# Performance work log

Measured on AMD Instinct MI355X. Metric: run time of the kernel, lower is better.

## Reference

```python
import jax, jax.numpy as jnp
import numpy as np

B, D, H, W = 4, 64, 64, 64
MODES = 8
WIDTH = 32
N_LAYERS = 4


def setup_inputs() -> dict:
    key = jax.random.key(0)
    ks = jax.random.split(key, 20)
    C = WIDTH
    m = MODES
    spec_scale = 1.0 / (C * C)
    inp = {
        "velocity_model": jax.random.normal(ks[0], (B, 1, D, H, W), jnp.float32),
        "partial_travel_time": jax.random.normal(ks[1], (B, 1, D, H, W), jnp.float32),
        "lift_w": jax.random.normal(ks[2], (2, C), jnp.float32) * 0.5,
        "lift_b": jax.random.normal(ks[3], (C,), jnp.float32) * 0.1,
        "spec_wr": jax.random.normal(ks[4], (N_LAYERS, 4, C, C, m, m, m), jnp.float32) * spec_scale,
        "spec_wi": jax.random.normal(ks[5], (N_LAYERS, 4, C, C, m, m, m), jnp.float32) * spec_scale,
        "skip_w": jax.random.normal(ks[6], (N_LAYERS, C, C), jnp.float32) * (1.0 / np.sqrt(C)),
        "skip_b": jax.random.normal(ks[7], (N_LAYERS, C), jnp.float32) * 0.1,
        "proj_w": jax.random.normal(ks[8], (C, C), jnp.float32) * (1.0 / np.sqrt(C)),
        "proj_b": jax.random.normal(ks[9], (C,), jnp.float32) * 0.1,
        "fc1_w": jax.random.normal(ks[10], (C, 128), jnp.float32) * (1.0 / np.sqrt(C)),
        "fc1_b": jax.random.normal(ks[11], (128,), jnp.float32) * 0.1,
        "fc2_w": jax.random.normal(ks[12], (128, 64), jnp.float32) * (1.0 / np.sqrt(128)),
        "fc2_b": jax.random.normal(ks[13], (64,), jnp.float32) * 0.1,
        "fc3_w": jax.random.normal(ks[14], (64, 3), jnp.float32) * (1.0 / np.sqrt(64)),
        "fc3_b": jax.random.normal(ks[15], (3,), jnp.float32) * 0.1,
    }
    return inp


def _spectral_conv3d(x, wr, wi, m):
    # x: [B, Cin, D, H, W] real; wr/wi: [4, Cin, Cout, m, m, m]
    b, ci, d, h, w = x.shape
    co = wr.shape[2]
    xf = jnp.fft.rfftn(x, axes=(-3, -2, -1))  # [B, Cin, D, H, W//2+1] complex
    wc = wr + 1j * wi
    lo = slice(None, m)
    hi = slice(-m, None)
    corners = [(lo, lo), (lo, hi), (hi, lo), (hi, hi)]
    out = jnp.zeros((b, co, d, h, w // 2 + 1), dtype=xf.dtype)
    for i, (sd, sh) in enumerate(corners):
        blk = jnp.einsum('bixyz,ioxyz->boxyz', xf[:, :, sd, sh, :m], wc[i])
        out = out.at[:, :, sd, sh, :m].set(blk)
    return jnp.fft.irfftn(out, s=(d, h, w), axes=(-3, -2, -1))


def _channel_linear(x, w, bias):
    # x: [B, Cin, D, H, W]; w: [Cin, Cout]
    return jnp.einsum('bixyz,io->boxyz', x, w) + bias[None, :, None, None, None]


def reference(velocity_model, partial_travel_time, lift_w, lift_b, spec_wr, spec_wi,
              skip_w, skip_b, proj_w, proj_b, fc1_w, fc1_b, fc2_w, fc2_b, fc3_w, fc3_b):
    # concat along channel dim -> [B, 2, D, H, W]
    x = jnp.concatenate([velocity_model, partial_travel_time], axis=1)
    # lifting to hidden width
    x = _channel_linear(x, lift_w, lift_b)
    n_layers = spec_wr.shape[0]
    for l in range(n_layers):
        y = _spectral_conv3d(x, spec_wr[l], spec_wi[l], MODES)
        s = _channel_linear(x, skip_w[l], skip_b[l])
        x = y + s
        if l < n_layers - 1:
            x = jax.nn.gelu(x)
    # projection to out_channels = width
    x = _channel_linear(x, proj_w, proj_b)
    # global spatial mean -> [B, width]
    x = jnp.mean(x, axis=(-3, -2, -1))
    # MLP head: width -> 128 -> 64 -> 3
    x = jax.nn.relu(x @ fc1_w + fc1_b)
    x = jax.nn.relu(x @ fc2_w + fc2_b)
    return x @ fc3_w + fc3_b
```

## Files before the change

kernel.cpp:

```cpp
#include <hip/hip_runtime.h>
#include <math.h>

#define NSP 262144
static constexpr float TWO_PI_OVER_64 = 0.09817477042468103f;

__global__ __launch_bounds__(256) void k_fwd_wh2(const float* __restrict__ vel,
                                                 const float* __restrict__ ptt,
                                                 float2* __restrict__ VP2) {
  __shared__ float plane[64][65];
  __shared__ float2 A[64][8];
  __shared__ float2 tw[64];
  int t = threadIdx.x;
  if (t < 64) { float s, c; sincosf(TWO_PI_OVER_64 * t, &s, &c); tw[t] = make_float2(c, s); }
  int b = blockIdx.x >> 7, ch = (blockIdx.x >> 6) & 1, d = blockIdx.x & 63;
  const float4* src = (const float4*)((ch ? ptt : vel) + (size_t)b * NSP + d * 4096);
  for (int p = 0; p < 4; ++p) {
    int i = t + 256 * p;
    float4 v = src[i];
    int h = i >> 4, sg = (i & 15) * 4;
    plane[h][sg] = v.x; plane[h][sg + 1] = v.y; plane[h][sg + 2] = v.z; plane[h][sg + 3] = v.w;
  }
  __syncthreads();
  for (int p = 0; p < 2; ++p) {
    int o = t + 256 * p;
    int h = o >> 3, kw = o & 7;
    float re = 0.f, im = 0.f;
    for (int w = 0; w < 64; ++w) {
      float2 cs = tw[(kw * w) & 63];
      float v = plane[h][w];
      re += v * cs.x; im -= v * cs.y;
    }
    A[h][kw] = make_float2(re, im);
  }
  __syncthreads();
  if (t < 128) {
    int kh = t >> 3, kw = t & 7;
    int f = (kh < 8) ? kh : kh + 48;
    float re = 0.f, im = 0.f;
    for (int h = 0; h < 64; ++h) {
      float2 cs = tw[(h * f) & 63];
      float2 a = A[h][kw];
      re += a.x * cs.x + a.y * cs.y;
      im += a.y * cs.x - a.x * cs.y;
    }
    VP2[(size_t)blockIdx.x * 128 + t] = make_float2(re, im);
  }
}

__global__ __launch_bounds__(256) void k_fwd_d_lift(const float2* __restrict__ VP2,
                                                    const float* __restrict__ lw,
                                                    const float* __restrict__ lb,
                                                    float2* __restrict__ X3) {
  __shared__ float2 tile[2][64][8];
  __shared__ float2 F[2][16][8];
  __shared__ float2 tw[64];
  int t = threadIdx.x;
  if (t < 64) { float s, c; sincosf(TWO_PI_OVER_64 * t, &s, &c); tw[t] = make_float2(c, s); }
  int b = blockIdx.x >> 4, kh = blockIdx.x & 15;
  for (int p = 0; p < 4; ++p) {
    int i = t + 256 * p;
    int ch = i >> 9, dd = (i >> 3) & 63, kw = i & 7;
    tile[ch][dd][kw] = VP2[(size_t)((b * 2 + ch) * 64 + dd) * 128 + kh * 8 + kw];
  }
  __syncthreads();
  { int ch = t >> 7, kd = (t >> 3) & 15, kw = t & 7;
    int f = (kd < 8) ? kd : kd + 48;
    float re = 0.f, im = 0.f;
    for (int dd = 0; dd < 64; ++dd) {
      float2 cs = tw[(dd * f) & 63];
      float2 v = tile[ch][dd][kw];
      re += v.x * cs.x + v.y * cs.y;
      im += v.y * cs.x - v.x * cs.y;
    }
    F[ch][kd][kw] = make_float2(re, im); }
  __syncthreads();
  for (int p = 0; p < 16; ++p) {
    int o = t + 256 * p;
    int ci = o >> 7, kd = (o >> 3) & 15, kw = o & 7;
    float2 f0 = F[0][kd][kw], f1 = F[1][kd][kw];
    float w0 = lw[ci], w1 = lw[32 + ci];
    float2 v = make_float2(w0 * f0.x + w1 * f1.x, w0 * f0.y + w1 * f1.y);
    if (kh == 0 && kd == 0 && kw == 0) v.x += lb[ci] * 262144.f;
    X3[(size_t)(b * 32 + ci) * 2048 + kd * 128 + kh * 8 + kw] = v;
  }
}

__global__ __launch_bounds__(128) void k_fwd_h(const float2* __restrict__ X1,
                                               float2* __restrict__ X2) {
  __shared__ float2 tile[64][8];
  __shared__ float2 tw[64];
  int t = threadIdx.x;
  if (t < 64) { float s, c; sincosf(TWO_PI_OVER_64 * t, &s, &c); tw[t] = make_float2(c, s); }
  const float4* s4 = (const float4*)(X1 + (size_t)blockIdx.x * 512);
  float4* t4 = (float4*)tile;
  t4[t] = s4[t];
  t4[t + 128] = s4[t + 128];
  __syncthreads();
  int kh = t >> 3, k = t & 7;
  int f = (kh < 8) ? kh : kh + 48;
  float2 E = tw[f];
  float2 cur = make_float2(1.f, 0.f);
  float re = 0.f, im = 0.f;
#pragma unroll 8
  for (int h = 0; h < 64; ++h) {
    float2 v = tile[h][k];
    re += v.x * cur.x + v.y * cur.y;
    im += v.y * cur.x - v.x * cur.y;
    float cx = cur.x * E.x - cur.y * E.y;
    cur.y = cur.x * E.y + cur.y * E.x;
    cur.x = cx;
  }
  X2[(size_t)blockIdx.x * 128 + t] = make_float2(re, im);
}

__global__ __launch_bounds__(128) void k_fwd_d(const float2* __restrict__ X2,
                                               float2* __restrict__ X3) {
  __shared__ float2 tile[64][8];
  __shared__ float2 tw[64];
  int t = threadIdx.x;
  if (t < 64) { float s, c; sincosf(TWO_PI_OVER_64 * t, &s, &c); tw[t] = make_float2(c, s); }
  int kh = blockIdx.x & 15, bc = blockIdx.x >> 4;
  const float2* src = X2 + (size_t)bc * 8192 + kh * 8;
  for (int i = t; i < 512; i += 128) tile[i >> 3][i & 7] = src[(i >> 3) * 128 + (i & 7)];
  __syncthreads();
  int kd = t >> 3, k = t & 7;
  int f = (kd < 8) ? kd : kd + 48;
  float2 E = tw[f];
  float2 cur = make_float2(1.f, 0.f);
  float re = 0.f, im = 0.f;
#pragma unroll 8
  for (int d = 0; d < 64; ++d) {
    float2 v = tile[d][k];
    re += v.x * cur.x + v.y * cur.y;
    im += v.y * cur.x - v.x * cur.y;
    float cx = cur.x * E.x - cur.y * E.y;
    cur.y = cur.x * E.y + cur.y * E.x;
    cur.x = cx;
  }
  X3[(size_t)bc * 2048 + kd * 128 + kh * 8 + k] = make_float2(re, im);
}

__global__ __launch_bounds__(256) void k_mix(const float2* __restrict__ X3,
                                             const float* __restrict__ wr,
                                             const float* __restrict__ wi,
                                             float2* __restrict__ Y3) {
  __shared__ float2 xs[4][32][8];
  int t = threadIdx.x;
  int kd = blockIdx.x >> 4, kh = blockIdx.x & 15;
  for (int i = t; i < 1024; i += 256) {
    int b = i >> 8, ci = (i >> 3) & 31, k = i & 7;
    xs[b][ci][k] = X3[(size_t)(b * 32 + ci) * 2048 + kd * 128 + kh * 8 + k];
  }
  __syncthreads();
  int corner = ((kd >= 8) ? 2 : 0) + ((kh >= 8) ? 1 : 0);
  int md = kd & 7, mh = kh & 7;
  int co = t >> 3, k = t & 7;
  size_t wbase = (size_t)corner * 32 * 32 * 512 + (size_t)md * 64 + (size_t)mh * 8 + k;
  float ar0 = 0, ai0 = 0, ar1 = 0, ai1 = 0, ar2 = 0, ai2 = 0, ar3 = 0, ai3 = 0;
  for (int ci = 0; ci < 32; ++ci) {
    size_t o = wbase + (size_t)(ci * 32 + co) * 512;
    float wre = wr[o], wim = wi[o];
    float2 v0 = xs[0][ci][k], v1 = xs[1][ci][k];
    float2 v2 = xs[2][ci][k], v3 = xs[3][ci][k];
    ar0 += v0.x * wre - v0.y * wim;  ai0 += v0.x * wim + v0.y * wre;
    ar1 += v1.x * wre - v1.y * wim;  ai1 += v1.x * wim + v1.y * wre;
    ar2 += v2.x * wre - v2.y * wim;  ai2 += v2.x * wim + v2.y * wre;
    ar3 += v3.x * wre - v3.y * wim;  ai3 += v3.x * wim + v3.y * wre;
  }
  size_t obase = (size_t)kd * 128 + kh * 8 + k;
  Y3[(size_t)(0 * 32 + co) * 2048 + obase] = make_float2(ar0, ai0);
  Y3[(size_t)(1 * 32 + co) * 2048 + obase] = make_float2(ar1, ai1);
  Y3[(size_t)(2 * 32 + co) * 2048 + obase] = make_float2(ar2, ai2);
  Y3[(size_t)(3 * 32 + co) * 2048 + obase] = make_float2(ar3, ai3);
}

__global__ __launch_bounds__(256) void k_inv_dh(const float2* __restrict__ Y3,
                                                float2* __restrict__ Z2) {
  __shared__ float2 yt[2048];
  __shared__ float2 zd[4][16][8];
  __shared__ float2 tw[64];
  int t = threadIdx.x;
  if (t < 64) { float s, c; sincosf(TWO_PI_OVER_64 * t, &s, &c); tw[t] = make_float2(c, s); }
  int bc = blockIdx.x >> 4, d0 = (blockIdx.x & 15) * 4;
  const float4* y4 = (const float4*)(Y3 + (size_t)bc * 2048);
  float4* yt4 = (float4*)yt;
  for (int p = 0; p < 4; ++p) yt4[t + 256 * p] = y4[t + 256 * p];
  __syncthreads();
  const float sc = 1.f / 262144.f;
  for (int p = 0; p < 2; ++p) {
    int o = t + 256 * p;
    int dd = o >> 7, kh = (o >> 3) & 15, kw = o & 7;
    int d = d0 + dd;
    float re = 0.f, im = 0.f;
#pragma unroll
    for (int kd = 0; kd < 16; ++kd) {
      int f = (kd < 8) ? kd : kd + 48;
      float2 cs = tw[(d * f) & 63];
      float2 v = yt[kd * 128 + kh * 8 + kw];
      re += v.x * cs.x - v.y * cs.y;
      im += v.x * cs.y + v.y * cs.x;
    }
    zd[dd][kh][kw] = make_float2(re * sc, im * sc);
  }
  __syncthreads();
  for (int p = 0; p < 8; ++p) {
    int o = t + 256 * p;
    int dd = o >> 9, h = (o >> 3) & 63, kw = o & 7;
    float re = 0.f, im = 0.f;
#pragma unroll
    for (int kh = 0; kh < 16; ++kh) {
      int f = (kh < 8) ? kh : kh + 48;
      float2 cs = tw[(h * f) & 63];
      float2 v = zd[dd][kh][kw];
      re += v.x * cs.x - v.y * cs.y;
      im += v.x * cs.y + v.y * cs.x;
    }
    Z2[((size_t)bc * 64 + d0 + dd) * 512 + h * 8 + kw] = make_float2(re, im);
  }
}

template <int MODE>
__global__ __launch_bounds__(256, 4) void k_tail(
    const float2* __restrict__ S, const float* __restrict__ xin,
    const float* __restrict__ pttin, const float* __restrict__ lw,
    const float* __restrict__ lb, const float* __restrict__ skw,
    const float* __restrict__ skb, float* __restrict__ xout,
    float2* __restrict__ Sout, float* __restrict__ pr) {
  __shared__ float2 tws[64];
  __shared__ float2 zt[32][2][9];
  __shared__ float sw[(MODE == 0) ? 3 : 32][32];
  __shared__ float xt[(MODE == 0) ? 2 : 32][2][64];
  int t = threadIdx.x;
  if (t < 64) { float s, c; sincosf(TWO_PI_OVER_64 * t, &s, &c); tws[t] = make_float2(c, s); }
  int b = blockIdx.x >> 11, d = (blockIdx.x >> 5) & 63, h0 = (blockIdx.x & 31) * 2;
  {
    int co = t >> 3, hh = (t >> 2) & 1, q = t & 3;
    const float4* S4 = (const float4*)S;
    float4 v = S4[(size_t)((b * 32 + co) * 64 + d) * 256 + (h0 + hh) * 4 + q];
    zt[co][hh][2 * q] = make_float2(v.x, v.y);
    zt[co][hh][2 * q + 1] = make_float2(v.z, v.w);
  }
  if constexpr (MODE == 0) {
    if (t < 64) {
      int ch = t >> 5, hh = (t >> 4) & 1, sg = t & 15;
      const float4* src = (const float4*)(ch ? pttin : xin);
      *(float4*)&xt[ch][hh][sg * 4] =
          src[((size_t)b * NSP + d * 4096 + (h0 + hh) * 64) / 4 + sg];
    } else if (t >= 128 && t < 192) {
      int j = (t >> 5) & 1, co = t & 31;
      float a = 0.f;
      for (int ci = 0; ci < 32; ++ci) a += lw[j * 32 + ci] * skw[ci * 32 + co];
      sw[j][co] = a;
    } else if (t >= 192 && t < 224) {
      int co = t & 31;
      float a = skb[co];
      for (int ci = 0; ci < 32; ++ci) a += lb[ci] * skw[ci * 32 + co];
      sw[2][co] = a;
    }
  } else {
    { int ci = t >> 3, q = t & 7;
      *(float4*)&sw[ci][q * 4] = ((const float4*)skw)[t]; }
    for (int p = 0; p < 4; ++p) {
      int idx = t + 256 * p, row = idx >> 4, ci = row >> 1, hh = row & 1, sg = idx & 15;
      *(float4*)&xt[ci][hh][sg * 4] =
          ((const float4*)xin)[(size_t)(((b * 32 + ci) * 64 + d) * 64 + h0 + hh) * 16 + sg];
    }
  }
  __syncthreads();

  int co = t >> 3, ws = t & 7;
  float2 e1[8];
#pragma unroll
  for (int j = 0; j < 8; ++j) e1[j] = tws[8 * ws + j];
  float bias = (MODE == 0) ? sw[2][co] : skb[co];

  float acc[2][8];
  {
    float z00 = zt[co][0][0].x, z10 = zt[co][1][0].x;
#pragma unroll
    for (int j = 0; j < 8; ++j) { acc[0][j] = bias + z00; acc[1][j] = bias + z10; }
  }
  {
    float2 cur[8];
#pragma unroll
    for (int j = 0; j < 8; ++j) cur[j] = e1[j];
#pragma unroll
    for (int k = 1; k < 8; ++k) {
      float2 z0 = zt[co][0][k], z1 = zt[co][1][k];
#pragma unroll
      for (int j = 0; j < 8; ++j) {
        acc[0][j] += 2.f * (z0.x * cur[j].x - z0.y * cur[j].y);
        acc[1][j] += 2.f * (z1.x * cur[j].x - z1.y * cur[j].y);
      }
      if (k < 7)
#pragma unroll
        for (int j = 0; j < 8; ++j) {
          float cx = cur[j].x * e1[j].x - cur[j].y * e1[j].y;
          cur[j].y = cur[j].x * e1[j].y + cur[j].y * e1[j].x;
          cur[j].x = cx;
        }
    }
  }
  constexpr int NCI = (MODE == 0) ? 2 : 32;
#pragma unroll 4
  for (int ci = 0; ci < NCI; ++ci) {
    float s = sw[ci][co];
#pragma unroll
    for (int hh = 0; hh < 2; ++hh) {
      float4 xa = *(const float4*)&xt[ci][hh][8 * ws];
      float4 xb = *(const float4*)&xt[ci][hh][8 * ws + 4];
      acc[hh][0] += xa.x * s;  acc[hh][1] += xa.y * s;
      acc[hh][2] += xa.z * s;  acc[hh][3] += xa.w * s;
      acc[hh][4] += xb.x * s;  acc[hh][5] += xb.y * s;
      acc[hh][6] += xb.z * s;  acc[hh][7] += xb.w * s;
    }
  }
#pragma unroll
  for (int hh = 0; hh < 2; ++hh)
#pragma unroll
    for (int j = 0; j < 8; ++j) {
      float v = acc[hh][j];
      float u = 0.7978845608028654f * (v + 0.044715f * v * v * v);
      acc[hh][j] = __fdividef(v, 1.f + __expf(-2.f * u));
    }

  if constexpr (MODE == 2) {
    float s = 0.f;
#pragma unroll
    for (int hh = 0; hh < 2; ++hh)
#pragma unroll
      for (int j = 0; j < 8; ++j) s += acc[hh][j];
    s += __shfl_down(s, 4, 8);
    s += __shfl_down(s, 2, 8);
    s += __shfl_down(s, 1, 8);
    if (ws == 0) atomicAdd(&pr[b * 32 + co], s);
  } else {
    float4* x4o = (float4*)xout;
#pragma unroll
    for (int hh = 0; hh < 2; ++hh) {
      size_t o = (((size_t)(b * 32 + co) * 64 + d) * 64 + h0 + hh) * 16 + 2 * ws;
      x4o[o]     = make_float4(acc[hh][0], acc[hh][1], acc[hh][2], acc[hh][3]);
      x4o[o + 1] = make_float4(acc[hh][4], acc[hh][5], acc[hh][6], acc[hh][7]);
    }
    float2 P[2][8];
#pragma unroll
    for (int hh = 0; hh < 2; ++hh)
#pragma unroll
      for (int kw = 0; kw < 8; ++kw) P[hh][kw] = make_float2(0.f, 0.f);
#pragma unroll
    for (int j = 0; j < 8; ++j) {
      float2 cc = make_float2(e1[j].x, -e1[j].y);
      float2 cur = make_float2(1.f, 0.f);
      float g0 = acc[0][j], g1 = acc[1][j];
#pragma unroll
      for (int kw = 0; kw < 8; ++kw) {
        P[0][kw].x += g0 * cur.x;  P[0][kw].y += g0 * cur.y;
        P[1][kw].x += g1 * cur.x;  P[1][kw].y += g1 * cur.y;
        if (kw < 7) {
          float cx = cur.x * cc.x - cur.y * cc.y;
          cur.y = cur.x * cc.y + cur.y * cc.x;
          cur.x = cx;
        }
      }
    }
    float2 Q[2][4];
#pragma unroll
    for (int hh = 0; hh < 2; ++hh)
#pragma unroll
      for (int kk = 0; kk < 4; ++kk) {
        float2 keep = (ws & 4) ? P[hh][kk + 4] : P[hh][kk];
        float2 send = (ws & 4) ? P[hh][kk] : P[hh][kk + 4];
        keep.x += __shfl_xor(send.x, 4);
        keep.y += __shfl_xor(send.y, 4);
        Q[hh][kk] = keep;
      }
    float2 R[2][2];
#pragma unroll
    for (int hh = 0; hh < 2; ++hh)
#pragma unroll
      for (int kk = 0; kk < 2; ++kk) {
        float2 keep = (ws & 2) ? Q[hh][kk + 2] : Q[hh][kk];
        float2 send = (ws & 2) ? Q[hh][kk] : Q[hh][kk + 2];
        keep.x += __shfl_xor(send.x, 2);
        keep.y += __shfl_xor(send.y, 2);
        R[hh][kk] = keep;
      }
#pragma unroll
    for (int hh = 0; hh < 2; ++hh) {
      float2 keep = (ws & 1) ? R[hh][1] : R[hh][0];
      float2 send = (ws & 1) ? R[hh][0] : R[hh][1];
      keep.x += __shfl_xor(send.x, 1);
      keep.y += __shfl_xor(send.y, 1);
      Sout[((size_t)(b * 32 + co) * 64 + d) * 512 + (h0 + hh) * 8 + ws] = keep;
    }
  }
}

__global__ __launch_bounds__(128) void k_head(const float* __restrict__ pr,
                                              const float* __restrict__ swr,
                                              const float* __restrict__ skw,
                                              const float* __restrict__ skb,
                                              const float* __restrict__ pw,
                                              const float* __restrict__ pb,
                                              const float* __restrict__ f1w,
                                              const float* __restrict__ f1b,
                                              const float* __restrict__ f2w,
                                              const float* __restrict__ f2b,
                                              const float* __restrict__ f3w,
                                              const float* __restrict__ f3b,
                                              float* __restrict__ out) {
  __shared__ float m[128], h1[128], p2[128], f1[512], f2[256];
  int t = threadIdx.x;
  m[t] = pr[t] * (1.f / 262144.f);
  __syncthreads();
  { int b = t >> 5, co = t & 31;
    float acc = skb[96 + co];
    for (int ci = 0; ci < 32; ++ci) {
      float wdc = swr[((size_t)12 * 1024 + (size_t)(ci * 32 + co)) * 512];
      acc += m[b * 32 + ci] * (wdc + skw[3072 + ci * 32 + co]);
    }
    h1[t] = acc; }
  __syncthreads();
  { int b = t >> 5, o = t & 31;
    float acc = pb[o];
    for (int c = 0; c < 32; ++c) acc += h1[b * 32 + c] * pw[c * 32 + o];
    p2[t] = acc; }
  __syncthreads();
  for (int j = 0; j < 4; ++j) {
    int idx = t + 128 * j, b = idx >> 7, o = idx & 127;
    float acc = f1b[o];
    for (int c = 0; c < 32; ++c) acc += p2[b * 32 + c] * f1w[c * 128 + o];
    f1[idx] = fmaxf(acc, 0.f);
  }
  __syncthreads();
  for (int j = 0; j < 2; ++j) {
    int idx = t + 128 * j, b = idx >> 6, o = idx & 63;
    float acc = f2b[o];
    for (int c = 0; c < 128; ++c) acc += f1[b * 128 + c] * f2w[c * 64 + o];
    f2[idx] = fmaxf(acc, 0.f);
  }
  __syncthreads();
  if (t < 12) {
    int b = t / 3, o = t % 3;
    float acc = f3b[o];
    for (int c = 0; c < 64; ++c) acc += f2[b * 64 + c] * f3w[c * 3 + o];
    out[t] = acc;
  }
}

extern "C" void kernel_launch(void* const* d_in, const int* in_sizes, int n_in,
                              void* d_out, int out_size, void* d_ws, size_t ws_size,
                              hipStream_t stream) {
  const float* vel = (const float*)d_in[0];
  const float* ptt = (const float*)d_in[1];
  const float* lw  = (const float*)d_in[2];
  const float* lb  = (const float*)d_in[3];
  const float* swr = (const float*)d_in[4];
  const float* swi = (const float*)d_in[5];
  const float* skw = (const float*)d_in[6];
  const float* skb = (const float*)d_in[7];
  const float* pw  = (const float*)d_in[8];
  const float* pb  = (const float*)d_in[9];
  const float* f1w = (const float*)d_in[10];
  const float* f1b = (const float*)d_in[11];
  const float* f2w = (const float*)d_in[12];
  const float* f2b = (const float*)d_in[13];
  const float* f3w = (const float*)d_in[14];
  const float* f3b = (const float*)d_in[15];
  float* out = (float*)d_out;

  char* ws = (char*)d_ws;
  float*  x   = (float*)(ws);
  float2* S   = (float2*)(ws + 134217728ULL);
  float2* X2  = (float2*)(ws + 167772160ULL);
  float2* VP2 = X2;
  float2* X3  = (float2*)(ws + 176160768ULL);
  float2* Y3  = (float2*)(ws + 178257920ULL);
  float*  pr  = (float*)(ws + 180355072ULL);
  if (ws_size < 180355584ULL) return;

  hipMemsetAsync(pr, 0, 512, stream);

  k_fwd_wh2<<<512, 256, 0, stream>>>(vel, ptt, VP2);
  k_fwd_d_lift<<<64, 256, 0, stream>>>(VP2, lw, lb, X3);
  k_mix<<<256, 256, 0, stream>>>(X3, swr, swi, Y3);
  k_inv_dh<<<2048, 256, 0, stream>>>(Y3, S);
  k_tail<0><<<8192, 256, 0, stream>>>(S, vel, ptt, lw, lb, skw, skb, x, S, nullptr);

  k_fwd_h<<<8192, 128, 0, stream>>>(S, X2);
  k_fwd_d<<<2048, 128, 0, stream>>>(X2, X3);
  k_mix<<<256, 256, 0, stream>>>(X3, swr + 2097152, swi + 2097152, Y3);
  k_inv_dh<<<2048, 256, 0, stream>>>(Y3, S);
  k_tail<1><<<8192, 256, 0, stream>>>(S, x, nullptr, nullptr, nullptr,
                                      skw + 1024, skb + 32, x, S, nullptr);

  k_fwd_h<<<8192, 128, 0, stream>>>(S, X2);
  k_fwd_d<<<2048, 128, 0, stream>>>(X2, X3);
  k_mix<<<256, 256, 0, stream>>>(X3, swr + 2 * 2097152, swi + 2 * 2097152, Y3);
  k_inv_dh<<<2048, 256, 0, stream>>>(Y3, S);
  k_tail<2><<<8192, 256, 0, stream>>>(S, x, nullptr, nullptr, nullptr,
                                      skw + 2048, skb + 64, nullptr, nullptr, pr);

  k_head<<<1, 128, 0, stream>>>(pr, swr, skw, skb, pw, pb, f1w, f1b,
                                f2w, f2b, f3w, f3b, out);
}
```

Measured before the change: 738.1 us.

## Register-block k_tail over four output channels and use twiddle table lookups in forward DFTs

k_tail now runs 128 threads per block, with each thread computing four output channels for one h row instead of one channel for two rows. This reuses the x tile and twiddle values across more accumulators and halves the thread count. The forward H and D DFT kernels swap their recurrence-based twiddle rotation for direct shared-memory table lookups, which removes a serial dependency chain. The larger per-thread accumulator set raises register pressure, and the lower occupancy hint (3) may reduce latency hiding.

After: 1.015 ms. +37.5%, slower.

```diff
diff --git a/kernel.cpp b/kernel.cpp
--- a/kernel.cpp
+++ b/kernel.cpp
@@ -98,17 +98,13 @@
   __syncthreads();
   int kh = t >> 3, k = t & 7;
   int f = (kh < 8) ? kh : kh + 48;
-  float2 E = tw[f];
-  float2 cur = make_float2(1.f, 0.f);
   float re = 0.f, im = 0.f;
 #pragma unroll 8
   for (int h = 0; h < 64; ++h) {
+    float2 cs = tw[(h * f) & 63];
     float2 v = tile[h][k];
-    re += v.x * cur.x + v.y * cur.y;
-    im += v.y * cur.x - v.x * cur.y;
-    float cx = cur.x * E.x - cur.y * E.y;
-    cur.y = cur.x * E.y + cur.y * E.x;
-    cur.x = cx;
+    re += v.x * cs.x + v.y * cs.y;
+    im += v.y * cs.x - v.x * cs.y;
   }
   X2[(size_t)blockIdx.x * 128 + t] = make_float2(re, im);
 }
@@ -125,17 +121,13 @@
   __syncthreads();
   int kd = t >> 3, k = t & 7;
   int f = (kd < 8) ? kd : kd + 48;
-  float2 E = tw[f];
-  float2 cur = make_float2(1.f, 0.f);
   float re = 0.f, im = 0.f;
 #pragma unroll 8
   for (int d = 0; d < 64; ++d) {
+    float2 cs = tw[(d * f) & 63];
     float2 v = tile[d][k];
-    re += v.x * cur.x + v.y * cur.y;
-    im += v.y * cur.x - v.x * cur.y;
-    float cx = cur.x * E.x - cur.y * E.y;
-    cur.y = cur.x * E.y + cur.y * E.x;
-    cur.x = cx;
+    re += v.x * cs.x + v.y * cs.y;
+    im += v.y * cs.x - v.x * cs.y;
   }
   X3[(size_t)bc * 2048 + kd * 128 + kh * 8 + k] = make_float2(re, im);
 }
@@ -220,7 +212,7 @@
 }
 
 template <int MODE>
-__global__ __launch_bounds__(256, 4) void k_tail(
+__global__ __launch_bounds__(128, 3) void k_tail(
     const float2* __restrict__ S, const float* __restrict__ xin,
     const float* __restrict__ pttin, const float* __restrict__ lw,
     const float* __restrict__ lb, const float* __restrict__ skw,
@@ -234,11 +226,15 @@
   if (t < 64) { float s, c; sincosf(TWO_PI_OVER_64 * t, &s, &c); tws[t] = make_float2(c, s); }
   int b = blockIdx.x >> 11, d = (blockIdx.x >> 5) & 63, h0 = (blockIdx.x & 31) * 2;
   {
-    int co = t >> 3, hh = (t >> 2) & 1, q = t & 3;
+    int co = t >> 2, sub = t & 3;
     const float4* S4 = (const float4*)S;
-    float4 v = S4[(size_t)((b * 32 + co) * 64 + d) * 256 + (h0 + hh) * 4 + q];
-    zt[co][hh][2 * q] = make_float2(v.x, v.y);
-    zt[co][hh][2 * q + 1] = make_float2(v.z, v.w);
+    size_t base = (size_t)((b * 32 + co) * 64 + d) * 256;
+#pragma unroll
+    for (int hh = 0; hh < 2; ++hh) {
+      float4 v = S4[base + (h0 + hh) * 4 + sub];
+      zt[co][hh][2 * sub] = make_float2(v.x, v.y);
+      zt[co][hh][2 * sub + 1] = make_float2(v.z, v.w);
+    }
   }
   if constexpr (MODE == 0) {
     if (t < 64) {
@@ -246,39 +242,47 @@
       const float4* src = (const float4*)(ch ? pttin : xin);
       *(float4*)&xt[ch][hh][sg * 4] =
           src[((size_t)b * NSP + d * 4096 + (h0 + hh) * 64) / 4 + sg];
-    } else if (t >= 128 && t < 192) {
-      int j = (t >> 5) & 1, co = t & 31;
-      float a = 0.f;
-      for (int ci = 0; ci < 32; ++ci) a += lw[j * 32 + ci] * skw[ci * 32 + co];
-      sw[j][co] = a;
-    } else if (t >= 192 && t < 224) {
-      int co = t & 31;
-      float a = skb[co];
-      for (int ci = 0; ci < 32; ++ci) a += lb[ci] * skw[ci * 32 + co];
-      sw[2][co] = a;
+    } else {
+      for (int i = t - 64; i < 96; i += 64) {
+        int r = i >> 5, co = i & 31;
+        if (r < 2) {
+          float a = 0.f;
+          for (int ci = 0; ci < 32; ++ci) a += lw[r * 32 + ci] * skw[ci * 32 + co];
+          sw[r][co] = a;
+        } else {
+          float a = skb[co];
+          for (int ci = 0; ci < 32; ++ci) a += lb[ci] * skw[ci * 32 + co];
+          sw[2][co] = a;
+        }
+      }
     }
   } else {
-    { int ci = t >> 3, q = t & 7;
-      *(float4*)&sw[ci][q * 4] = ((const float4*)skw)[t]; }
-    for (int p = 0; p < 4; ++p) {
-      int idx = t + 256 * p, row = idx >> 4, ci = row >> 1, hh = row & 1, sg = idx & 15;
+    ((float4*)sw)[t] = ((const float4*)skw)[t];
+    ((float4*)sw)[t + 128] = ((const float4*)skw)[t + 128];
+    for (int p = 0; p < 8; ++p) {
+      int idx = t + 128 * p, row = idx >> 4, ci = row >> 1, hh = row & 1, sg = idx & 15;
       *(float4*)&xt[ci][hh][sg * 4] =
           ((const float4*)xin)[(size_t)(((b * 32 + ci) * 64 + d) * 64 + h0 + hh) * 16 + sg];
     }
   }
   __syncthreads();
 
-  int co = t >> 3, ws = t & 7;
+  int cog = t >> 4, hh = (t >> 3) & 1, ws = t & 7;
+  int co0 = cog * 4;
   float2 e1[8];
 #pragma unroll
   for (int j = 0; j < 8; ++j) e1[j] = tws[8 * ws + j];
-  float bias = (MODE == 0) ? sw[2][co] : skb[co];
-
-  float acc[2][8];
-  {
-    float z00 = zt[co][0][0].x, z10 = zt[co][1][0].x;
-#pragma unroll
-    for (int j = 0; j < 8; ++j) { acc[0][j] = bias + z00; acc[1][j] = bias + z10; }
+  float bias[4];
+#pragma unroll
+  for (int r = 0; r < 4; ++r)
+    bias[r] = (MODE == 0) ? sw[2][co0 + r] : skb[co0 + r];
+
+  float acc[4][8];
+#pragma unroll
+  for (int r = 0; r < 4; ++r) {
+    float z0 = zt[co0 + r][hh][0].x + bias[r];
+#pragma unroll
+    for (int j = 0; j < 8; ++j) acc[r][j] = z0;
   }
   {
     float2 cur[8];
@@ -286,12 +290,14 @@
     for (int j = 0; j < 8; ++j) cur[j] = e1[j];
 #pragma unroll
     for (int k = 1; k < 8; ++k) {
-      float2 z0 = zt[co][0][k], z1 = zt[co][1][k];
-#pragma unroll
-      for (int j = 0; j < 8; ++j) {
-        acc[0][j] += 2.f * (z0.x * cur[j].x - z0.y * cur[j].y);
-        acc[1][j] += 2.f * (z1.x * cur[j].x - z1.y * cur[j].y);
-      }
+      float2 z[4];
+#pragma unroll
+      for (int r = 0; r < 4; ++r) z[r] = zt[co0 + r][hh][k];
+#pragma unroll
+      for (int r = 0; r < 4; ++r)
+#pragma unroll
+        for (int j = 0; j < 8; ++j)
+          acc[r][j] += 2.f * (z[r].x * cur[j].x - z[r].y * cur[j].y);
       if (k < 7)
 #pragma unroll
         for (int j = 0; j < 8; ++j) {
@@ -304,94 +310,102 @@
   constexpr int NCI = (MODE == 0) ? 2 : 32;
 #pragma unroll 4
   for (int ci = 0; ci < NCI; ++ci) {
-    float s = sw[ci][co];
-#pragma unroll
-    for (int hh = 0; hh < 2; ++hh) {
-      float4 xa = *(const float4*)&xt[ci][hh][8 * ws];
-      float4 xb = *(const float4*)&xt[ci][hh][8 * ws + 4];
-      acc[hh][0] += xa.x * s;  acc[hh][1] += xa.y * s;
-      acc[hh][2] += xa.z * s;  acc[hh][3] += xa.w * s;
-      acc[hh][4] += xb.x * s;  acc[hh][5] += xb.y * s;
-      acc[hh][6] += xb.z * s;  acc[hh][7] += xb.w * s;
-    }
-  }
-#pragma unroll
-  for (int hh = 0; hh < 2; ++hh)
+    float4 sv = *(const float4*)&sw[ci][co0];
+    float4 xa = *(const float4*)&xt[ci][hh][8 * ws];
+    float4 xb = *(const float4*)&xt[ci][hh][8 * ws + 4];
+    float xv[8] = {xa.x, xa.y, xa.z, xa.w, xb.x, xb.y, xb.z, xb.w};
+    float svv[4] = {sv.x, sv.y, sv.z, sv.w};
+#pragma unroll
+    for (int r = 0; r < 4; ++r)
+#pragma unroll
+      for (int j = 0; j < 8; ++j) acc[r][j] += xv[j] * svv[r];
+  }
+#pragma unroll
+  for (int r = 0; r < 4; ++r)
 #pragma unroll
     for (int j = 0; j < 8; ++j) {
-      float v = acc[hh][j];
+      float v = acc[r][j];
       float u = 0.7978845608028654f * (v + 0.044715f * v * v * v);
-      acc[hh][j] = __fdividef(v, 1.f + __expf(-2.f * u));
+      acc[r][j] = __fdividef(v, 1.f + __expf(-2.f * u));
     }
 
   if constexpr (MODE == 2) {
-    float s = 0.f;
-#pragma unroll
-    for (int hh = 0; hh < 2; ++hh)
-#pragma unroll
-      for (int j = 0; j < 8; ++j) s += acc[hh][j];
-    s += __shfl_down(s, 4, 8);
-    s += __shfl_down(s, 2, 8);
-    s += __shfl_down(s, 1, 8);
-    if (ws == 0) atomicAdd(&pr[b * 32 + co], s);
+    float rs[4];
+#pragma unroll
+    for (int r = 0; r < 4; ++r) {
+      float s = 0.f;
+#pragma unroll
+      for (int j = 0; j < 8; ++j) s += acc[r][j];
+      rs[r] = s;
+    }
+#pragma unroll
+    for (int off = 1; off < 16; off <<= 1)
+#pragma unroll
+      for (int r = 0; r < 4; ++r) rs[r] += __shfl_xor(rs[r], off);
+    if ((t & 15) == 0)
+#pragma unroll
+      for (int r = 0; r < 4; ++r) atomicAdd(&pr[b * 32 + co0 + r], rs[r]);
   } else {
     float4* x4o = (float4*)xout;
 #pragma unroll
-    for (int hh = 0; hh < 2; ++hh) {
-      size_t o = (((size_t)(b * 32 + co) * 64 + d) * 64 + h0 + hh) * 16 + 2 * ws;
-      x4o[o]     = make_float4(acc[hh][0], acc[hh][1], acc[hh][2], acc[hh][3]);
-      x4o[o + 1] = make_float4(acc[hh][4], acc[hh][5], acc[hh][6], acc[hh][7]);
-    }
-    float2 P[2][8];
-#pragma unroll
-    for (int hh = 0; hh < 2; ++hh)
-#pragma unroll
-      for (int kw = 0; kw < 8; ++kw) P[hh][kw] = make_float2(0.f, 0.f);
-#pragma unroll
-    for (int j = 0; j < 8; ++j) {
-      float2 cc = make_float2(e1[j].x, -e1[j].y);
-      float2 cur = make_float2(1.f, 0.f);
-      float g0 = acc[0][j], g1 = acc[1][j];
-#pragma unroll
-      for (int kw = 0; kw < 8; ++kw) {
-        P[0][kw].x += g0 * cur.x;  P[0][kw].y += g0 * cur.y;
-        P[1][kw].x += g1 * cur.x;  P[1][kw].y += g1 * cur.y;
-        if (kw < 7) {
-          float cx = cur.x * cc.x - cur.y * cc.y;
-          cur.y = cur.x * cc.y + cur.y * cc.x;
-          cur.x = cx;
+    for (int r = 0; r < 4; ++r) {
+      size_t o = (((size_t)(b * 32 + co0 + r) * 64 + d) * 64 + h0 + hh) * 16 + 2 * ws;
+      x4o[o]     = make_float4(acc[r][0], acc[r][1], acc[r][2], acc[r][3]);
+      x4o[o + 1] = make_float4(acc[r][4], acc[r][5], acc[r][6], acc[r][7]);
+    }
+#pragma unroll
+    for (int half = 0; half < 2; ++half) {
+      float2 P[2][8];
+#pragma unroll
+      for (int rr = 0; rr < 2; ++rr)
+#pragma unroll
+        for (int kw = 0; kw < 8; ++kw) P[rr][kw] = make_float2(0.f, 0.f);
+#pragma unroll
+      for (int j = 0; j < 8; ++j) {
+        float2 cc = make_float2(e1[j].x, -e1[j].y);
+        float2 cur = make_float2(1.f, 0.f);
+        float g0 = acc[2 * half][j], g1 = acc[2 * half + 1][j];
+#pragma unroll
+        for (int kw = 0; kw < 8; ++kw) {
+          P[0][kw].x += g0 * cur.x;  P[0][kw].y += g0 * cur.y;
+          P[1][kw].x += g1 * cur.x;  P[1][kw].y += g1 * cur.y;
+          if (kw < 7) {
+            float cx = cur.x * cc.x - cur.y * cc.y;
+            cur.y = cur.x * cc.y + cur.y * cc.x;
+            cur.x = cx;
+          }
         }
       }
-    }
-    float2 Q[2][4];
-#pragma unroll
-    for (int hh = 0; hh < 2; ++hh)
-#pragma unroll
-      for (int kk = 0; kk < 4; ++kk) {
-        float2 keep = (ws & 4) ? P[hh][kk + 4] : P[hh][kk];
-        float2 send = (ws & 4) ? P[hh][kk] : P[hh][kk + 4];
-        keep.x += __shfl_xor(send.x, 4);
-        keep.y += __shfl_xor(send.y, 4);
-        Q[hh][kk] = keep;
+      float2 Q[2][4];
+#pragma unroll
+      for (int rr = 0; rr < 2; ++rr)
+#pragma unroll
+        for (int kk = 0; kk < 4; ++kk) {
+          float2 keep = (ws & 4) ? P[rr][kk + 4] : P[rr][kk];
+          float2 send = (ws & 4) ? P[rr][kk] : P[rr][kk + 4];
+          keep.x += __shfl_xor(send.x, 4);
+          keep.y += __shfl_xor(send.y, 4);
+          Q[rr][kk] = keep;
+        }
+      float2 R[2][2];
+#pragma unroll
+      for (int rr = 0; rr < 2; ++rr)
+#pragma unroll
+        for (int kk = 0; kk < 2; ++kk) {
+          float2 keep = (ws & 2) ? Q[rr][kk + 2] : Q[rr][kk];
+          float2 send = (ws & 2) ? Q[rr][kk] : Q[rr][kk + 2];
+          keep.x += __shfl_xor(send.x, 2);
+          keep.y += __shfl_xor(send.y, 2);
+          R[rr][kk] = keep;
+        }
+#pragma unroll
+      for (int rr = 0; rr < 2; ++rr) {
+        float2 keep = (ws & 1) ? R[rr][1] : R[rr][0];
+        float2 send = (ws & 1) ? R[rr][0] : R[rr][1];
+        keep.x += __shfl_xor(send.x, 1);
+        keep.y += __shfl_xor(send.y, 1);
+        Sout[((size_t)(b * 32 + co0 + 2 * half + rr) * 64 + d) * 512 + (h0 + hh) * 8 + ws] = keep;
       }
-    float2 R[2][2];
-#pragma unroll
-    for (int hh = 0; hh < 2; ++hh)
-#pragma unroll
-      for (int kk = 0; kk < 2; ++kk) {
-        float2 keep = (ws & 2) ? Q[hh][kk + 2] : Q[hh][kk];
-        float2 send = (ws & 2) ? Q[hh][kk] : Q[hh][kk + 2];
-        keep.x += __shfl_xor(send.x, 2);
-        keep.y += __shfl_xor(send.y, 2);
-        R[hh][kk] = keep;
-      }
-#pragma unroll
-    for (int hh = 0; hh < 2; ++hh) {
-      float2 keep = (ws & 1) ? R[hh][1] : R[hh][0];
-      float2 send = (ws & 1) ? R[hh][0] : R[hh][1];
-      keep.x += __shfl_xor(send.x, 1);
-      keep.y += __shfl_xor(send.y, 1);
-      Sout[((size_t)(b * 32 + co) * 64 + d) * 512 + (h0 + hh) * 8 + ws] = keep;
     }
   }
 }
@@ -485,20 +499,20 @@
   k_fwd_d_lift<<<64, 256, 0, stream>>>(VP2, lw, lb, X3);
   k_mix<<<256, 256, 0, stream>>>(X3, swr, swi, Y3);
   k_inv_dh<<<2048, 256, 0, stream>>>(Y3, S);
-  k_tail<0><<<8192, 256, 0, stream>>>(S, vel, ptt, lw, lb, skw, skb, x, S, nullptr);
+  k_tail<0><<<8192, 128, 0, stream>>>(S, vel, ptt, lw, lb, skw, skb, x, S, nullptr);
 
   k_fwd_h<<<8192, 128, 0, stream>>>(S, X2);
   k_fwd_d<<<2048, 128, 0, stream>>>(X2, X3);
   k_mix<<<256, 256, 0, stream>>>(X3, swr + 2097152, swi + 2097152, Y3);
   k_inv_dh<<<2048, 256, 0, stream>>>(Y3, S);
-  k_tail<1><<<8192, 256, 0, stream>>>(S, x, nullptr, nullptr, nullptr,
+  k_tail<1><<<8192, 128, 0, stream>>>(S, x, nullptr, nullptr, nullptr,
                                       skw + 1024, skb + 32, x, S, nullptr);
 
   k_fwd_h<<<8192, 128, 0, stream>>>(S, X2);
   k_fwd_d<<<2048, 128, 0, stream>>>(X2, X3);
   k_mix<<<256, 256, 0, stream>>>(X3, swr + 2 * 2097152, swi + 2 * 2097152, Y3);
   k_inv_dh<<<2048, 256, 0, stream>>>(Y3, S);
-  k_tail<2><<<8192, 256, 0, stream>>>(S, x, nullptr, nullptr, nullptr,
+  k_tail<2><<<8192, 128, 0, stream>>>(S, x, nullptr, nullptr, nullptr,
                                       skw + 2048, skb + 64, nullptr, nullptr, pr);
 
   k_head<<<1, 128, 0, stream>>>(pr, swr, skw, skb, pw, pb, f1w, f1b,
```
